# Optimization experiments

Hardware: AMD Instinct MI355X
Metric: run time of the kernel (lower is better)

Reference implementation:

```python
import jax, jax.numpy as jnp
import numpy as np

B, T, C = 4, 2048, 2048
N_HEAD, N_HEAD_KV = 16, 4
HEAD_DIM = C // N_HEAD
ROPE_BASE = 10000.0


def setup_inputs() -> dict:
    key = jax.random.key(0)
    ks = jax.random.split(key, 6)
    x = jax.random.normal(ks[0], (B, T, C), dtype=jnp.float32)
    # freqs_cis: (T, head_dim//2, 2) with [...,0]=cos, [...,1]=sin (true RoPE angles)
    inv_freq = 1.0 / (ROPE_BASE ** (jnp.arange(0, HEAD_DIM, 2, dtype=jnp.float32) / HEAD_DIM))
    angles = jnp.arange(T, dtype=jnp.float32)[:, None] * inv_freq[None, :]  # (T, hd//2)
    freqs_cis = jnp.stack([jnp.cos(angles), jnp.sin(angles)], axis=-1)
    s = 0.02
    Wq = jax.random.normal(ks[1], (C, C), dtype=jnp.float32) * s
    Wk = jax.random.normal(ks[2], (N_HEAD_KV * HEAD_DIM, C), dtype=jnp.float32) * s
    Wv = jax.random.normal(ks[3], (N_HEAD_KV * HEAD_DIM, C), dtype=jnp.float32) * s
    Wo = jax.random.normal(ks[4], (C, C), dtype=jnp.float32) * s
    return {"x": x, "freqs_cis": freqs_cis, "Wq": Wq, "Wk": Wk, "Wv": Wv, "Wo": Wo}


def _rotate_half(u):
    h = u.shape[-1] // 2
    return jnp.concatenate([-u[..., h:], u[..., :h]], axis=-1)


def reference(x, freqs_cis, Wq, Wk, Wv, Wo):
    b, t, c = x.shape
    hd = HEAD_DIM
    q = (x @ Wq.T).reshape(b, t, N_HEAD, hd)
    k = (x @ Wk.T).reshape(b, t, N_HEAD_KV, hd)
    v = (x @ Wv.T).reshape(b, t, N_HEAD_KV, hd)
    # external RoPE (3-dim freqs_cis): cos/sin repeated to full head_dim
    cos = freqs_cis[:t, :, 0]
    sin = freqs_cis[:t, :, 1]
    cos = jnp.concatenate([cos, cos], axis=-1)[None, :, None, :]  # (1,T,1,hd)
    sin = jnp.concatenate([sin, sin], axis=-1)[None, :, None, :]
    q = q * cos + _rotate_half(q) * sin
    k = k * cos + _rotate_half(k) * sin
    # GQA: repeat_interleave kv heads to n_head
    g = N_HEAD // N_HEAD_KV
    k = jnp.repeat(k, g, axis=2)  # (B,T,H,hd)
    v = jnp.repeat(v, g, axis=2)
    scale = 1.0 / np.sqrt(hd)
    scores = jnp.einsum('bthd,bshd->bhts', q, k) * scale  # (B,H,T,S)
    causal = jnp.tril(jnp.ones((t, t), dtype=bool))
    neg = jnp.finfo(scores.dtype).min
    scores = jnp.where(causal[None, None, :, :], scores, neg)
    attn = jax.nn.softmax(scores, axis=-1)
    out = jnp.einsum('bhts,bshd->bthd', attn, v).reshape(b, t, c)
    return out @ Wo.T
```

## Files before the change

kernel.cpp:

```cpp
#include <hip/hip_runtime.h>
#include <hip/hip_bf16.h>
#include <stdint.h>

typedef __bf16 bf16_t;
typedef __bf16 bf16x4 __attribute__((ext_vector_type(4)));
typedef __bf16 bf16x8 __attribute__((ext_vector_type(8)));
typedef float f32x4 __attribute__((ext_vector_type(4)));

__device__ __forceinline__ float fast_exp2(float x) {
#if __has_builtin(__builtin_amdgcn_exp2f)
  return __builtin_amdgcn_exp2f(x);
#else
  return exp2f(x);
#endif
}

__global__ void cvt_all(const float* __restrict__ x,  const float* __restrict__ Wq,
                        const float* __restrict__ Wk, const float* __restrict__ Wv,
                        const float* __restrict__ Wo, bf16_t* __restrict__ xb,
                        bf16_t* __restrict__ wqkv, bf16_t* __restrict__ wob) {
  const int bid = blockIdx.x, tid = threadIdx.x;
  const float* src; bf16_t* dst; int i;
  if (bid < 16384)      { src = x;  dst = xb;             i = bid * 256 + tid; }
  else if (bid < 20480) { src = Wq; dst = wqkv;           i = (bid - 16384) * 256 + tid; }
  else if (bid < 21504) { src = Wk; dst = wqkv + 4194304; i = (bid - 20480) * 256 + tid; }
  else if (bid < 22528) { src = Wv; dst = wqkv + 5242880; i = (bid - 21504) * 256 + tid; }
  else                  { src = Wo; dst = wob;            i = (bid - 22528) * 256 + tid; }
  float4 v = ((const float4*)src)[i];
  bf16x4 o = { (bf16_t)v.x, (bf16_t)v.y, (bf16_t)v.z, (bf16_t)v.w };
  *(bf16x4*)(dst + (size_t)i * 4) = o;
}

__device__ __forceinline__ void async_load16(const bf16_t* g, bf16_t* l) {
#if __has_builtin(__builtin_amdgcn_global_load_lds)
  __builtin_amdgcn_global_load_lds((const __attribute__((address_space(1))) void*)g,
                                   (__attribute__((address_space(3))) void*)l, 16, 0, 0);
#else
  *(bf16x8*)l = *(const bf16x8*)g;
#endif
}

template<bool F32OUT, bool VSPLIT>
__global__ __launch_bounds__(512, 2) void gemm256(const bf16_t* __restrict__ A,
                                                  const bf16_t* __restrict__ B,
                                                  void* __restrict__ C,
                                                  bf16_t* __restrict__ Vt,
                                                  int NBN, int K, int ldc) {
  __shared__ bf16_t As[2][256 * 64];
  __shared__ bf16_t Bs[2][256 * 64];
  const int tid = threadIdx.x;
  const int wave = tid >> 6, lane = tid & 63;
  const int lrow = lane & 15, quad = lane >> 4;
  const int wr = wave >> 2, wc = wave & 3;
  const int nwg = gridDim.x;
  const int wg  = (blockIdx.x & 7) * (nwg >> 3) + (blockIdx.x >> 3);
  const int bm = wg / NBN, bn = wg % NBN;
  const bf16_t* Ag = A + (size_t)bm * 256 * K;
  const bf16_t* Bg = B + (size_t)bn * 256 * K;
  const int srow = tid >> 3;
  const int schunk = (tid & 7) ^ (srow & 7);

  f32x4 acc[2][2][4][2] = {};
  bf16x8 af[4][2], bfr[2][2];
  const int NT = K >> 6;

  auto stageA = [&](int mh, int bsel, int kk) {
#pragma unroll
    for (int i = 0; i < 2; ++i)
      async_load16(Ag + (size_t)(mh * 128 + i * 64 + srow) * K + kk + schunk * 8,
                   &As[bsel][mh * 8192 + i * 4096 + tid * 8]);
  };
  auto stageB = [&](int nh, int bsel, int kk) {
#pragma unroll
    for (int i = 0; i < 2; ++i)
      async_load16(Bg + (size_t)(nh * 128 + i * 64 + srow) * K + kk + schunk * 8,
                   &Bs[bsel][nh * 8192 + i * 4096 + tid * 8]);
  };

#define READ_A(MH)                                                                   \
  _Pragma("unroll")                                                                  \
  for (int mfi = 0; mfi < 4; ++mfi) {                                                \
    const int ra = (MH) * 128 + mfi * 32 + wr * 16 + lrow;                           \
    _Pragma("unroll")                                                                \
    for (int ks = 0; ks < 2; ++ks)                                                   \
      af[mfi][ks] = *(const bf16x8*)&As[buf][ra * 64 +                               \
                        (((ks * 4 + quad) ^ (lrow & 7)) << 3)];                      \
  }
#define READ_B(NH)                                                                   \
  _Pragma("unroll")                                                                  \
  for (int nfi = 0; nfi < 2; ++nfi) {                                                \
    const int rb = (NH) * 128 + nfi * 64 + wc * 16 + lrow;                           \
    _Pragma("unroll")                                                                \
    for (int ks = 0; ks < 2; ++ks)                                                   \
      bfr[nfi][ks] = *(const bf16x8*)&Bs[buf][rb * 64 +                              \
                         (((ks * 4 + quad) ^ (lrow & 7)) << 3)];                     \
  }
#define MFMA_Q(MH, NH)                                                               \
  __builtin_amdgcn_s_setprio(1);                                                     \
  _Pragma("unroll")                                                                  \
  for (int ks = 0; ks < 2; ++ks)                                                     \
    _Pragma("unroll")                                                                \
    for (int mfi = 0; mfi < 4; ++mfi)                                                \
      _Pragma("unroll")                                                              \
      for (int nfi = 0; nfi < 2; ++nfi)                                              \
        acc[MH][NH][mfi][nfi] = __builtin_amdgcn_mfma_f32_16x16x32_bf16(             \
            af[mfi][ks], bfr[nfi][ks], acc[MH][NH][mfi][nfi], 0, 0, 0);              \
  __builtin_amdgcn_s_setprio(0);

  stageA(0, 0, 0);
  stageB(0, 0, 0);
  stageB(1, 0, 0);
  stageA(1, 0, 0);
  asm volatile("s_waitcnt vmcnt(4)" ::: "memory");
  __builtin_amdgcn_s_barrier();

  for (int t = 0; t < NT; ++t) {
    const int buf = t & 1, obuf = buf ^ 1;
    const int kn = (t + 1) << 6;
    const bool pf = (t + 1 < NT);
    READ_A(0)
    READ_B(0)
    if (pf) stageA(0, obuf, kn);
    __builtin_amdgcn_s_barrier();
    asm volatile("s_waitcnt lgkmcnt(0)" ::: "memory");
    MFMA_Q(0, 0)
    if (pf) asm volatile("s_waitcnt vmcnt(4)" ::: "memory");
    else    asm volatile("s_waitcnt vmcnt(2)" ::: "memory");
    __builtin_amdgcn_s_barrier();
    READ_B(1)
    if (pf) stageB(0, obuf, kn);
    __builtin_amdgcn_s_barrier();
    asm volatile("s_waitcnt lgkmcnt(0)" ::: "memory");
    MFMA_Q(0, 1)
    if (pf) asm volatile("s_waitcnt vmcnt(4)" ::: "memory");
    else    asm volatile("s_waitcnt vmcnt(0)" ::: "memory");
    __builtin_amdgcn_s_barrier();
    READ_A(1)
    if (pf) stageB(1, obuf, kn);
    __builtin_amdgcn_s_barrier();
    asm volatile("s_waitcnt lgkmcnt(0)" ::: "memory");
    MFMA_Q(1, 1)
    __builtin_amdgcn_s_barrier();
    READ_B(0)
    if (pf) stageA(1, obuf, kn);
    __builtin_amdgcn_s_barrier();
    asm volatile("s_waitcnt lgkmcnt(0)" ::: "memory");
    MFMA_Q(1, 0)
    if (pf) asm volatile("s_waitcnt vmcnt(4)" ::: "memory");
    __builtin_amdgcn_s_barrier();
  }
#undef READ_A
#undef READ_B
#undef MFMA_Q

  if (VSPLIT && bn >= 10) {
#pragma unroll
    for (int mh = 0; mh < 2; ++mh)
#pragma unroll
      for (int nh = 0; nh < 2; ++nh)
#pragma unroll
        for (int mfi = 0; mfi < 4; ++mfi)
#pragma unroll
          for (int nfi = 0; nfi < 2; ++nfi) {
            int row = bm * 256 + mh * 128 + mfi * 32 + wr * 16 + quad * 4;
            int cv  = bn * 256 + nh * 128 + nfi * 64 + wc * 16 + lrow - 2560;
            int b = row >> 11, tl = row & 2047;
            bf16x4 o;
#pragma unroll
            for (int r = 0; r < 4; ++r) o[r] = (bf16_t)acc[mh][nh][mfi][nfi][r];
            *(bf16x4*)&Vt[((size_t)(b * 512 + cv)) * 2048 + tl] = o;
          }
    return;
  }
#pragma unroll
  for (int mh = 0; mh < 2; ++mh)
#pragma unroll
    for (int nh = 0; nh < 2; ++nh)
#pragma unroll
      for (int mfi = 0; mfi < 4; ++mfi)
#pragma unroll
        for (int nfi = 0; nfi < 2; ++nfi)
#pragma unroll
          for (int r = 0; r < 4; ++r) {
            int row = bm * 256 + mh * 128 + mfi * 32 + wr * 16 + quad * 4 + r;
            int col = bn * 256 + nh * 128 + nfi * 64 + wc * 16 + lrow;
            if (F32OUT) ((float*)C)[(size_t)row * ldc + col] = acc[mh][nh][mfi][nfi][r];
            else        ((bf16_t*)C)[(size_t)row * ldc + col] = (bf16_t)acc[mh][nh][mfi][nfi][r];
          }
}

__global__ void rope_kernel(bf16_t* __restrict__ X, const float* __restrict__ F,
                            int hshift, int stride) {
  int i = blockIdx.x * blockDim.x + threadIdx.x;
  int d = i & 63;
  int h = (i >> 6) & ((1 << hshift) - 1);
  int row = i >> (6 + hshift);
  int t = row & 2047;
  float c = F[t * 128 + d * 2];
  float s = F[t * 128 + d * 2 + 1];
  size_t base = (size_t)row * stride + h * 128 + d;
  float q0 = (float)X[base];
  float q1 = (float)X[base + 64];
  X[base]      = (bf16_t)(q0 * c - q1 * s);
  X[base + 64] = (bf16_t)(q1 * c + q0 * s);
}

__global__ __launch_bounds__(256, 2) void attn_kernel(const bf16_t* __restrict__ QKV,
                                                      const float* __restrict__ F,
                                                      const bf16_t* __restrict__ Vt,
                                                      bf16_t* __restrict__ O) {
  __shared__ bf16_t Ks[2][64 * 128];
  __shared__ bf16_t Vs[2][128 * 64];
  __shared__ bf16_t Ps[4 * 32 * 64];
  const int tid = threadIdx.x;
  const int wave = tid >> 6, lane = tid & 63;
  const int lrow = lane & 15, quad = lane >> 4;
  const int bh = blockIdx.y, b = bh >> 4, h = bh & 15, kvh = h >> 2;
  const size_t qoff  = ((size_t)b * 2048) * 2560 + (size_t)h * 128;
  const size_t koff  = ((size_t)b * 2048) * 2560 + 2048 + (size_t)kvh * 128;
  const size_t vtoff = ((size_t)(b * 4 + kvh) * 128) * 2048;
  const float qsc = 0.08838834764831845f * 1.44269504088896340736f;
  bf16_t* Pw = Ps + wave * (32 * 64);
  const float2* F2 = (const float2*)F;

  const int krow_l = tid >> 4;
  const int kdc    = (tid & 15) ^ (krow_l & 7);
  const int vrow_l = tid >> 3;
  const int vkc    = (tid & 7) ^ (vrow_l & 7);

  auto stage = [&](int kt, int bsel) {
    const bf16_t* Kg = QKV + koff + (size_t)(kt * 64) * 2560;
    const bf16_t* Vg = Vt + vtoff + kt * 64;
    bf16_t* Kd = &Ks[bsel][0];
    bf16_t* Vd = &Vs[bsel][0];
#pragma unroll
    for (int c4 = 0; c4 < 4; ++c4) {
      int ci = c4 * 256 + tid;
      async_load16(Kg + (size_t)(c4 * 16 + krow_l) * 2560 + kdc * 8, Kd + ci * 8);
      async_load16(Vg + (size_t)(c4 * 32 + vrow_l) * 2048 + vkc * 8, Vd + ci * 8);
    }
  };

  for (int phase = 0; phase < 2; ++phase) {
    const int qt = phase ? (15 - blockIdx.x) : blockIdx.x;
    const int qbase = qt * 128 + wave * 32;

    bf16x8 qf[2][4];
#pragma unroll
    for (int nt2 = 0; nt2 < 2; ++nt2) {
      const int t = qbase + nt2 * 16 + lrow;
      const bf16_t* qp = QKV + qoff + (size_t)t * 2560 + quad * 8;
      bf16x8 raw[4];
#pragma unroll
      for (int ks = 0; ks < 4; ++ks) raw[ks] = *(const bf16x8*)(qp + ks * 32);
#pragma unroll
      for (int ks2 = 0; ks2 < 2; ++ks2) {
        bf16x8 lo, hi;
#pragma unroll
        for (int j = 0; j < 8; ++j) {
          int d = ks2 * 32 + quad * 8 + j;
          float2 cs = F2[t * 64 + d];
          float q0 = (float)raw[ks2][j], q1 = (float)raw[ks2 + 2][j];
          lo[j] = (bf16_t)((q0 * cs.x - q1 * cs.y) * qsc);
          hi[j] = (bf16_t)((q1 * cs.x + q0 * cs.y) * qsc);
        }
        qf[nt2][ks2]     = lo;
        qf[nt2][ks2 + 2] = hi;
      }
    }

    f32x4 Oacc[2][8] = {};
    float m_r[2] = {-1.0e30f, -1.0e30f};
    float l_r[2] = {0.f, 0.f};
    const int kt_end = 2 * qt + 2;

    stage(0, 0);

    for (int kt = 0; kt < kt_end; ++kt) {
      __syncthreads();
      if (kt + 1 < kt_end) stage(kt + 1, (kt + 1) & 1);
      const bf16_t* Kb_ = &Ks[kt & 1][0];
      const bf16_t* Vb_ = &Vs[kt & 1][0];

      if (kt * 64 <= qbase + 31) {
        f32x4 S[2][4] = {};
#pragma unroll
        for (int ks = 0; ks < 4; ++ks) {
          bf16x8 kf[4];
#pragma unroll
          for (int mt = 0; mt < 4; ++mt) {
            int dc = (ks * 4 + quad) ^ (lrow & 7);
            kf[mt] = *(const bf16x8*)&Kb_[(mt * 16 + lrow) * 128 + dc * 8];
          }
#pragma unroll
          for (int nt2 = 0; nt2 < 2; ++nt2)
#pragma unroll
            for (int mt = 0; mt < 4; ++mt)
              S[nt2][mt] = __builtin_amdgcn_mfma_f32_16x16x32_bf16(kf[mt], qf[nt2][ks], S[nt2][mt], 0, 0, 0);
        }
        if (kt * 64 + 63 > qbase) {
#pragma unroll
          for (int nt2 = 0; nt2 < 2; ++nt2) {
            int q = qbase + nt2 * 16 + lrow;
#pragma unroll
            for (int mt = 0; mt < 4; ++mt) {
              int key0 = kt * 64 + mt * 16 + quad * 4;
#pragma unroll
              for (int r = 0; r < 4; ++r)
                if (key0 + r > q) S[nt2][mt][r] = -1.0e30f;
            }
          }
        }
        float alpha[2];
#pragma unroll
        for (int nt2 = 0; nt2 < 2; ++nt2) {
          float mx = -1.0e30f;
#pragma unroll
          for (int mt = 0; mt < 4; ++mt)
#pragma unroll
            for (int r = 0; r < 4; ++r) mx = fmaxf(mx, S[nt2][mt][r]);
          mx = fmaxf(mx, __shfl_xor(mx, 16, 64));
          mx = fmaxf(mx, __shfl_xor(mx, 32, 64));
          float mnew = fmaxf(m_r[nt2], mx);
          alpha[nt2] = fast_exp2(m_r[nt2] - mnew);
          m_r[nt2] = mnew;
          float rs = 0.f;
          const int prow = nt2 * 16 + lrow;
          const int pbase = prow * 64 + ((quad & 1) << 2);
#pragma unroll
          for (int mt = 0; mt < 4; ++mt) {
            bf16x4 pk;
#pragma unroll
            for (int r = 0; r < 4; ++r) {
              float p = fast_exp2(S[nt2][mt][r] - mnew);
              rs += p;
              pk[r] = (bf16_t)p;
            }
            int c8 = ((mt * 2 + (quad >> 1)) ^ (prow & 7)) << 3;
            *(bf16x4*)&Pw[pbase + c8] = pk;
          }
          rs += __shfl_xor(rs, 16, 64);
          rs += __shfl_xor(rs, 32, 64);
          l_r[nt2] = l_r[nt2] * alpha[nt2] + rs;
        }
        bool nz = (alpha[0] != 1.f) || (alpha[1] != 1.f);
        if (__ballot(nz) != 0ull) {
#pragma unroll
          for (int mt2 = 0; mt2 < 2; ++mt2)
#pragma unroll
            for (int r = 0; r < 4; ++r) {
              float av = __shfl(alpha[mt2], quad * 4 + r, 16);
#pragma unroll
              for (int dt = 0; dt < 8; ++dt) Oacc[mt2][dt][r] *= av;
            }
        }
#pragma unroll
        for (int ks2 = 0; ks2 < 2; ++ks2) {
          bf16x8 ap[2];
#pragma unroll
          for (int mt2 = 0; mt2 < 2; ++mt2) {
            int prow = mt2 * 16 + lrow;
            ap[mt2] = *(const bf16x8*)&Pw[prow * 64 + (((ks2 * 4 + quad) ^ (prow & 7)) << 3)];
          }
          int dc = (ks2 * 4 + quad) ^ (lrow & 7);
#pragma unroll
          for (int dt = 0; dt < 8; ++dt) {
            bf16x8 bv = *(const bf16x8*)&Vb_[(dt * 16 + lrow) * 64 + dc * 8];
#pragma unroll
            for (int mt2 = 0; mt2 < 2; ++mt2)
              Oacc[mt2][dt] = __builtin_amdgcn_mfma_f32_16x16x32_bf16(ap[mt2], bv, Oacc[mt2][dt], 0, 0, 0);
          }
        }
      }
    }

#pragma unroll
    for (int mt2 = 0; mt2 < 2; ++mt2)
#pragma unroll
      for (int r = 0; r < 4; ++r) {
        float lv = __shfl(l_r[mt2], quad * 4 + r, 16);
        float inv = 1.0f / lv;
        int row = qbase + mt2 * 16 + quad * 4 + r;
#pragma unroll
        for (int dt = 0; dt < 8; ++dt)
          O[(size_t)b * 2048 * 2048 + (size_t)row * 2048 + h * 128 + dt * 16 + lrow] =
              (bf16_t)(Oacc[mt2][dt][r] * inv);
      }
  }
}

extern "C" void kernel_launch(void* const* d_in, const int* in_sizes, int n_in,
                              void* d_out, int out_size, void* d_ws, size_t ws_size,
                              hipStream_t stream) {
  const float* x  = (const float*)d_in[0];
  const float* fc = (const float*)d_in[1];
  const float* Wq = (const float*)d_in[2];
  const float* Wk = (const float*)d_in[3];
  const float* Wv = (const float*)d_in[4];
  const float* Wo = (const float*)d_in[5];
  float* out = (float*)d_out;

  char* ws = (char*)d_ws;
  size_t off = 0;
  auto alloc = [&](size_t bytes) { char* p = ws + off; off += bytes; return p; };
  bf16_t* xb    = (bf16_t*)alloc((size_t)8192 * 2048 * 2);
  bf16_t* Wqkvb = (bf16_t*)alloc((size_t)3072 * 2048 * 2);
  bf16_t* Wob   = (bf16_t*)alloc((size_t)2048 * 2048 * 2);
  bf16_t* QKVb  = (bf16_t*)alloc((size_t)8192 * 2560 * 2);
  bf16_t* Ab    = (bf16_t*)alloc((size_t)8192 * 2048 * 2);
  bf16_t* Vtb   = (bf16_t*)alloc((size_t)2048 * 2048 * 2);
  (void)ws_size; (void)in_sizes; (void)n_in; (void)out_size;

  cvt_all<<<26624, 256, 0, stream>>>(x, Wq, Wk, Wv, Wo, xb, Wqkvb, Wob);

  gemm256<false, true><<<384, 512, 0, stream>>>(xb, Wqkvb, QKVb, Vtb, 12, 2048, 2560);

  rope_kernel<<<8192, 256, 0, stream>>>(QKVb + 2048, fc, 2, 2560);

  attn_kernel<<<dim3(8, 64), 256, 0, stream>>>(QKVb, fc, Vtb, Ab);

  gemm256<true, false><<<256, 512, 0, stream>>>(Ab, Wob, out, nullptr, 8, 2048, 2048);
}
```

Before: 463.2 us.

## Replace QKV GEMM with 128x128 single-buffered kernel and lazy softmax max rescaling

Adds a simpler gemm_bt kernel with 128x128 tiles, 256 threads and a single LDS buffer, and uses it for the QKV projection in place of the double-buffered 256x256 gemm256. Separately, the attention softmax now keeps the old running max unless the new block max exceeds it by more than 8 (in log2 units), which skips rescaling work. The new GEMM gives up the double-buffer overlap and larger tile reuse in exchange for more blocks and better occupancy. Lazy max updates can let exponentials reach up to 2^8, which slightly raises the risk of bf16 precision loss in P.

```diff
diff --git a/kernel.cpp b/kernel.cpp
--- a/kernel.cpp
+++ b/kernel.cpp
@@ -38,6 +38,79 @@
 #else
   *(bf16x8*)l = *(const bf16x8*)g;
 #endif
+}
+
+template<bool F32OUT, bool VSPLIT>
+__global__ __launch_bounds__(256) void gemm_bt(const bf16_t* __restrict__ A,
+                                               const bf16_t* __restrict__ B,
+                                               void* __restrict__ C,
+                                               bf16_t* __restrict__ Vt,
+                                               int M, int N, int K, int ldc) {
+  __shared__ bf16_t Alds[128 * 64];
+  __shared__ bf16_t Blds[128 * 64];
+  const int tid = threadIdx.x;
+  const int wave = tid >> 6, lane = tid & 63;
+  const int lrow = lane & 15, quad = lane >> 4;
+  const int wr = wave >> 1, wc = wave & 1;
+  const int bm = blockIdx.y, bn = blockIdx.x;
+  const bf16_t* Ab = A + (size_t)bm * 128 * K;
+  const bf16_t* Bb = B + (size_t)bn * 128 * K;
+  const int r0 = tid >> 3;
+  const int c0 = ((tid & 7) ^ (r0 & 7)) << 3;
+  f32x4 acc[4][4] = {};
+
+  for (int kk = 0; kk < K; kk += 64) {
+#pragma unroll
+    for (int p = 0; p < 4; ++p) {
+      async_load16(Ab + (size_t)(p * 32 + r0) * K + kk + c0, &Alds[(p * 256 + tid) * 8]);
+      async_load16(Bb + (size_t)(p * 32 + r0) * K + kk + c0, &Blds[(p * 256 + tid) * 8]);
+    }
+    __syncthreads();
+#pragma unroll
+    for (int ks2 = 0; ks2 < 2; ++ks2) {
+      const int rc = ((ks2 * 4 + quad) ^ (lrow & 7)) << 3;
+      bf16x8 af[4], bfv[4];
+#pragma unroll
+      for (int mt = 0; mt < 4; ++mt)
+        af[mt] = *(const bf16x8*)&Alds[(wr * 64 + mt * 16 + lrow) * 64 + rc];
+#pragma unroll
+      for (int nt = 0; nt < 4; ++nt)
+        bfv[nt] = *(const bf16x8*)&Blds[(wc * 64 + nt * 16 + lrow) * 64 + rc];
+#pragma unroll
+      for (int mt = 0; mt < 4; ++mt)
+#pragma unroll
+        for (int nt = 0; nt < 4; ++nt)
+          acc[mt][nt] = __builtin_amdgcn_mfma_f32_16x16x32_bf16(af[mt], bfv[nt], acc[mt][nt], 0, 0, 0);
+    }
+    __syncthreads();
+  }
+
+  if (VSPLIT && bn >= 20) {
+#pragma unroll
+    for (int mt = 0; mt < 4; ++mt)
+#pragma unroll
+      for (int nt = 0; nt < 4; ++nt) {
+        int row = bm * 128 + wr * 64 + mt * 16 + quad * 4;
+        int cv  = bn * 128 + wc * 64 + nt * 16 + lrow - 2560;
+        int b = row >> 11, tl = row & 2047;
+        bf16x4 o;
+#pragma unroll
+        for (int r = 0; r < 4; ++r) o[r] = (bf16_t)acc[mt][nt][r];
+        *(bf16x4*)&Vt[((size_t)(b * 512 + cv)) * 2048 + tl] = o;
+      }
+    return;
+  }
+#pragma unroll
+  for (int mt = 0; mt < 4; ++mt)
+#pragma unroll
+    for (int nt = 0; nt < 4; ++nt)
+#pragma unroll
+      for (int r = 0; r < 4; ++r) {
+        int row = bm * 128 + wr * 64 + mt * 16 + quad * 4 + r;
+        int col = bn * 128 + wc * 64 + nt * 16 + lrow;
+        if (F32OUT) ((float*)C)[(size_t)row * ldc + col] = acc[mt][nt][r];
+        else        ((bf16_t*)C)[(size_t)row * ldc + col] = (bf16_t)acc[mt][nt][r];
+      }
 }
 
 template<bool F32OUT, bool VSPLIT>
@@ -321,8 +394,9 @@
             for (int r = 0; r < 4; ++r) mx = fmaxf(mx, S[nt2][mt][r]);
           mx = fmaxf(mx, __shfl_xor(mx, 16, 64));
           mx = fmaxf(mx, __shfl_xor(mx, 32, 64));
-          float mnew = fmaxf(m_r[nt2], mx);
-          alpha[nt2] = fast_exp2(m_r[nt2] - mnew);
+          float mold = m_r[nt2];
+          float mnew = (mx - mold <= 8.0f) ? mold : mx;
+          alpha[nt2] = fast_exp2(mold - mnew);
           m_r[nt2] = mnew;
           float rs = 0.f;
           const int prow = nt2 * 16 + lrow;
@@ -413,7 +487,8 @@
 
   cvt_all<<<26624, 256, 0, stream>>>(x, Wq, Wk, Wv, Wo, xb, Wqkvb, Wob);
 
-  gemm256<false, true><<<384, 512, 0, stream>>>(xb, Wqkvb, QKVb, Vtb, 12, 2048, 2560);
+  gemm_bt<false, true><<<dim3(24, 64), 256, 0, stream>>>(xb, Wqkvb, QKVb, Vtb,
+                                                         8192, 3072, 2048, 2560);
 
   rope_kernel<<<8192, 256, 0, stream>>>(QKVb + 2048, fc, 2, 2560);
 
```

Result: faster. 430.9 us (-7.0%).
